# Optimization experiments

Hardware: AMD Instinct MI355X
Metric: run time of the kernel (lower is better)

Reference implementation:

```python
import jax, jax.numpy as jnp
import numpy as np

N_HEADS = 8


def setup_inputs() -> dict:
    key = jax.random.key(0)
    qkv = jax.random.normal(key, (4, 1536, 2048), dtype=jnp.float32)
    return {"qkv": qkv}


def reference(qkv):
    bs, width, length = qkv.shape
    assert width % (3 * N_HEADS) == 0
    ch = width // (3 * N_HEADS)
    q, k, v = jnp.split(qkv, 3, axis=1)            # each [bs, H*C, T]
    scale = 1.0 / (ch ** 0.25)                      # 1/sqrt(sqrt(ch)) applied to both q and k
    q = (q * scale).reshape(bs * N_HEADS, ch, length)
    k = (k * scale).reshape(bs * N_HEADS, ch, length)
    v = v.reshape(bs * N_HEADS, ch, length)
    weight = jnp.einsum('bct,bcs->bts', q, k)       # [bs*H, T, T]
    weight = jax.nn.softmax(weight.astype(jnp.float32), axis=-1).astype(weight.dtype)
    a = jnp.einsum('bts,bcs->bct', weight, v)       # [bs*H, C, T]
    return a.reshape(bs, -1, length)
```

## Files before the change

kernel.cpp:

```cpp
#include <hip/hip_runtime.h>


typedef _Float16 half8  __attribute__((ext_vector_type(8)));
typedef _Float16 half4  __attribute__((ext_vector_type(4)));
typedef float    floatx4 __attribute__((ext_vector_type(4)));

constexpr int T    = 2048;
constexpr int TQ   = 128;
constexpr int TS   = 64;
constexpr int LDK  = 72;
constexpr int LDV  = 72;
constexpr int KHALF  = TS * LDK;
constexpr int SMEM_H = KHALF + 64 * LDV;
constexpr int NIT  = T / TS;
constexpr float QSCALE = 0.125f * 1.44269504088896340736f;

__device__ __forceinline__ half4 pack4(float a, float b, float c, float d) {
    half4 r;
    r[0] = (_Float16)a; r[1] = (_Float16)b;
    r[2] = (_Float16)c; r[3] = (_Float16)d;
    return r;
}

__global__ __launch_bounds__(512, 4)
void qkv_attn_kernel(const float* __restrict__ qkv, float* __restrict__ out) {
    __shared__ __align__(16) _Float16 smem[2][SMEM_H];

    const int tid  = threadIdx.x;
    const int wave = tid >> 6;
    const int lane = tid & 63;
    const int n16  = lane & 15;
    const int g    = lane >> 4;
    const int h    = wave >> 2;
    const int qg   = wave & 3;

    const int bx = blockIdx.x;
    const int hd = bx & 31;
    const int qt = bx >> 5;
    const int b  = hd >> 3;
    const int hh = hd & 7;
    const int q0 = qt * TQ;

    const float* __restrict__ qbase = qkv + (size_t)(b * 1536 + hh * 64) * T;
    const float* __restrict__ kbase = qkv + (size_t)(b * 1536 + 512 + hh * 64) * T;
    const float* __restrict__ vbase = qkv + (size_t)(b * 1536 + 1024 + hh * 64) * T;
    float* __restrict__ obase = out + (size_t)(b * 512 + hh * 64) * T;

    const bool kstage = (wave < 4);
    const int ptid = tid & 255;
    const int ks   = ((ptid >> 6) << 4) | (ptid & 15);
    const int kc4  = ((ptid >> 4) & 3) << 2;
    const int vc   = ptid >> 4;
    const int vt   = ptid & 15;
    const int vcol = 32 * (vt >> 3) + 8 * (vt & 3) + 4 * ((vt >> 2) & 1);

    float pre[16];
    auto prefetch = [&](int s0) {
        if (kstage) {
            const float* kg = kbase + s0 + ks;
#pragma unroll
            for (int i = 0; i < 4; ++i) {
                const int c = i * 16 + kc4;
#pragma unroll
                for (int j = 0; j < 4; ++j) pre[i * 4 + j] = kg[(c + j) * T];
            }
        } else {
            const float* vg = vbase + vc * T + s0 + vt * 4;
#pragma unroll
            for (int i = 0; i < 4; ++i) {
                const floatx4 vv = *(const floatx4*)&vg[i * 16 * T];
                pre[i * 4 + 0] = vv.x; pre[i * 4 + 1] = vv.y;
                pre[i * 4 + 2] = vv.z; pre[i * 4 + 3] = vv.w;
            }
        }
    };
    auto flush = [&](int buf) {
        if (kstage) {
            _Float16* kd = &smem[buf][ks * LDK];
#pragma unroll
            for (int i = 0; i < 4; ++i)
                *(half4*)&kd[i * 16 + kc4] =
                    pack4(pre[i * 4], pre[i * 4 + 1], pre[i * 4 + 2], pre[i * 4 + 3]);
        } else {
            _Float16* vd = &smem[buf][KHALF + vc * LDV + vcol];
#pragma unroll
            for (int i = 0; i < 4; ++i)
                *(half4*)&vd[i * 16 * LDV] =
                    pack4(pre[i * 4], pre[i * 4 + 1], pre[i * 4 + 2], pre[i * 4 + 3]);
        }
    };

    half8 bq[2][2];
    floatx4 oacc[4][2];
    float lsum[2];

#pragma unroll
    for (int qt2 = 0; qt2 < 2; ++qt2) {
        const int q = q0 + qg * 32 + qt2 * 16 + n16;
#pragma unroll
        for (int kcA = 0; kcA < 2; ++kcA)
#pragma unroll
            for (int j = 0; j < 8; ++j) {
                const int c = kcA * 32 + g * 8 + j;
                bq[qt2][kcA][j] = (_Float16)(qbase[c * T + q] * QSCALE);
            }
    }
#pragma unroll
    for (int mt = 0; mt < 4; ++mt)
#pragma unroll
        for (int qt2 = 0; qt2 < 2; ++qt2) oacc[mt][qt2] = (floatx4)(0.f);
    lsum[0] = 0.f; lsum[1] = 0.f;

    prefetch(0);
    flush(0);
    __syncthreads();

    for (int it = 0; it < NIT; ++it) {
        const int buf = it & 1;
        if (it + 1 < NIT) prefetch((it + 1) * TS);

        const _Float16* kb = &smem[buf][0];
        const _Float16* vb = &smem[buf][KHALF];

        floatx4 sacc[2][2];
#pragma unroll
        for (int sub = 0; sub < 2; ++sub) {
            const half8 ak0 = *(const half8*)&kb[((h * 2 + sub) * 16 + n16) * LDK + g * 8];
            const half8 ak1 = *(const half8*)&kb[((h * 2 + sub) * 16 + n16) * LDK + 32 + g * 8];
#pragma unroll
            for (int qt2 = 0; qt2 < 2; ++qt2) {
                floatx4 acc = (floatx4)(0.f);
                acc = __builtin_amdgcn_mfma_f32_16x16x32_f16(ak0, bq[qt2][0], acc, 0, 0, 0);
                acc = __builtin_amdgcn_mfma_f32_16x16x32_f16(ak1, bq[qt2][1], acc, 0, 0, 0);
                sacc[qt2][sub] = acc;
            }
        }
        half8 av[4];
#pragma unroll
        for (int mt = 0; mt < 4; ++mt)
            av[mt] = *(const half8*)&vb[(mt * 16 + n16) * LDV + h * 32 + g * 8];
#pragma unroll
        for (int qt2 = 0; qt2 < 2; ++qt2) {
            float pv[8];
#pragma unroll
            for (int sub = 0; sub < 2; ++sub)
#pragma unroll
                for (int r = 0; r < 4; ++r)
                    pv[sub * 4 + r] = __builtin_amdgcn_exp2f(sacc[qt2][sub][r]);
            lsum[qt2] += ((pv[0] + pv[1]) + (pv[2] + pv[3]))
                       + ((pv[4] + pv[5]) + (pv[6] + pv[7]));
            half8 bp;
#pragma unroll
            for (int i = 0; i < 8; ++i) bp[i] = (_Float16)pv[i];
#pragma unroll
            for (int mt = 0; mt < 4; ++mt)
                oacc[mt][qt2] = __builtin_amdgcn_mfma_f32_16x16x32_f16(
                    av[mt], bp, oacc[mt][qt2], 0, 0, 0);
        }

        if (it + 1 < NIT) flush(buf ^ 1);
        __syncthreads();
    }

    float* red = (float*)&smem[0][0];
    const int rbase = (qg * 64 + lane) * 36;
    if (h == 1) {
#pragma unroll
        for (int qt2 = 0; qt2 < 2; ++qt2)
#pragma unroll
            for (int mt = 0; mt < 4; ++mt)
                *(floatx4*)&red[rbase + (qt2 * 4 + mt) * 4] = oacc[mt][qt2];
        red[rbase + 32] = lsum[0];
        red[rbase + 33] = lsum[1];
    }
    __syncthreads();
    if (h == 0) {
#pragma unroll
        for (int qt2 = 0; qt2 < 2; ++qt2)
#pragma unroll
            for (int mt = 0; mt < 4; ++mt)
                oacc[mt][qt2] += *(const floatx4*)&red[rbase + (qt2 * 4 + mt) * 4];
        lsum[0] += red[rbase + 32];
        lsum[1] += red[rbase + 33];
#pragma unroll
        for (int qt2 = 0; qt2 < 2; ++qt2) {
            float l = lsum[qt2];
            l += __shfl_xor(l, 16);
            l += __shfl_xor(l, 32);
            const float linv = 1.0f / l;
            const int tcol = q0 + qg * 32 + qt2 * 16 + n16;
#pragma unroll
            for (int mt = 0; mt < 4; ++mt)
#pragma unroll
                for (int r = 0; r < 4; ++r)
                    obase[(mt * 16 + g * 4 + r) * T + tcol] = oacc[mt][qt2][r] * linv;
        }
    }
}

extern "C" void kernel_launch(void* const* d_in, const int* in_sizes, int n_in,
                              void* d_out, int out_size, void* d_ws, size_t ws_size,
                              hipStream_t stream) {
    const float* qkv = (const float*)d_in[0];
    float* out = (float*)d_out;
    qkv_attn_kernel<<<dim3(512), dim3(512), 0, stream>>>(qkv, out);
}
```

Before: 124.3 us.

## Split keys four ways per block with 1024 threads and tree-reduce partials

Doubles the block to 1024 threads and the key tile to 128, so four wave groups each handle a quarter of every key tile for the same 128 queries. Partial outputs and row sums are then combined in a two-step shared-memory tree with an XOR swizzle. Staging now loads from global and writes straight into the other shared buffer, replacing the register prefetch and the flush after compute, and V fragments are loaded inside the MFMA loop to save registers. The aim is more waves in flight to hide latency, but it costs extra reduction barriers, global-load latency exposed before compute, and register pressure from the launch bounds.

```diff
diff --git a/kernel.cpp b/kernel.cpp
--- a/kernel.cpp
+++ b/kernel.cpp
@@ -7,12 +7,13 @@
 
 constexpr int T    = 2048;
 constexpr int TQ   = 128;
-constexpr int TS   = 64;
+constexpr int TS   = 128;
 constexpr int LDK  = 72;
-constexpr int LDV  = 72;
+constexpr int LDV  = 136;
 constexpr int KHALF  = TS * LDK;
 constexpr int SMEM_H = KHALF + 64 * LDV;
 constexpr int NIT  = T / TS;
+constexpr int LBASE = 16384;
 constexpr float QSCALE = 0.125f * 1.44269504088896340736f;
 
 __device__ __forceinline__ half4 pack4(float a, float b, float c, float d) {
@@ -22,7 +23,7 @@
     return r;
 }
 
-__global__ __launch_bounds__(512, 4)
+__global__ __launch_bounds__(1024, 8)
 void qkv_attn_kernel(const float* __restrict__ qkv, float* __restrict__ out) {
     __shared__ __align__(16) _Float16 smem[2][SMEM_H];
 
@@ -31,8 +32,8 @@
     const int lane = tid & 63;
     const int n16  = lane & 15;
     const int g    = lane >> 4;
-    const int h    = wave >> 2;
     const int qg   = wave & 3;
+    const int sq   = wave >> 2;
 
     const int bx = blockIdx.x;
     const int hd = bx & 31;
@@ -46,47 +47,35 @@
     const float* __restrict__ vbase = qkv + (size_t)(b * 1536 + 1024 + hh * 64) * T;
     float* __restrict__ obase = out + (size_t)(b * 512 + hh * 64) * T;
 
-    const bool kstage = (wave < 4);
-    const int ptid = tid & 255;
+    const bool kstage = (wave < 8);
+    const int ptid = tid & 511;
     const int ks   = ((ptid >> 6) << 4) | (ptid & 15);
     const int kc4  = ((ptid >> 4) & 3) << 2;
-    const int vc   = ptid >> 4;
-    const int vt   = ptid & 15;
+    const int vc   = ptid >> 5;
+    const int vt   = ptid & 31;
     const int vcol = 32 * (vt >> 3) + 8 * (vt & 3) + 4 * ((vt >> 2) & 1);
 
-    float pre[16];
-    auto prefetch = [&](int s0) {
+    auto stage = [&](int buf, int s0) {
         if (kstage) {
+            _Float16* kd = &smem[buf][ks * LDK];
             const float* kg = kbase + s0 + ks;
 #pragma unroll
             for (int i = 0; i < 4; ++i) {
                 const int c = i * 16 + kc4;
-#pragma unroll
-                for (int j = 0; j < 4; ++j) pre[i * 4 + j] = kg[(c + j) * T];
+                const float f0 = kg[(c + 0) * T];
+                const float f1 = kg[(c + 1) * T];
+                const float f2 = kg[(c + 2) * T];
+                const float f3 = kg[(c + 3) * T];
+                *(half4*)&kd[c] = pack4(f0, f1, f2, f3);
             }
         } else {
             const float* vg = vbase + vc * T + s0 + vt * 4;
+            _Float16* vd = &smem[buf][KHALF + vc * LDV + vcol];
 #pragma unroll
             for (int i = 0; i < 4; ++i) {
                 const floatx4 vv = *(const floatx4*)&vg[i * 16 * T];
-                pre[i * 4 + 0] = vv.x; pre[i * 4 + 1] = vv.y;
-                pre[i * 4 + 2] = vv.z; pre[i * 4 + 3] = vv.w;
-            }
-        }
-    };
-    auto flush = [&](int buf) {
-        if (kstage) {
-            _Float16* kd = &smem[buf][ks * LDK];
-#pragma unroll
-            for (int i = 0; i < 4; ++i)
-                *(half4*)&kd[i * 16 + kc4] =
-                    pack4(pre[i * 4], pre[i * 4 + 1], pre[i * 4 + 2], pre[i * 4 + 3]);
-        } else {
-            _Float16* vd = &smem[buf][KHALF + vc * LDV + vcol];
-#pragma unroll
-            for (int i = 0; i < 4; ++i)
-                *(half4*)&vd[i * 16 * LDV] =
-                    pack4(pre[i * 4], pre[i * 4 + 1], pre[i * 4 + 2], pre[i * 4 + 3]);
+                *(half4*)&vd[i * 16 * LDV] = pack4(vv.x, vv.y, vv.z, vv.w);
+            }
         }
     };
 
@@ -111,13 +100,12 @@
         for (int qt2 = 0; qt2 < 2; ++qt2) oacc[mt][qt2] = (floatx4)(0.f);
     lsum[0] = 0.f; lsum[1] = 0.f;
 
-    prefetch(0);
-    flush(0);
+    stage(0, 0);
     __syncthreads();
 
     for (int it = 0; it < NIT; ++it) {
         const int buf = it & 1;
-        if (it + 1 < NIT) prefetch((it + 1) * TS);
+        if (it + 1 < NIT) stage(buf ^ 1, (it + 1) * TS);
 
         const _Float16* kb = &smem[buf][0];
         const _Float16* vb = &smem[buf][KHALF];
@@ -125,8 +113,9 @@
         floatx4 sacc[2][2];
 #pragma unroll
         for (int sub = 0; sub < 2; ++sub) {
-            const half8 ak0 = *(const half8*)&kb[((h * 2 + sub) * 16 + n16) * LDK + g * 8];
-            const half8 ak1 = *(const half8*)&kb[((h * 2 + sub) * 16 + n16) * LDK + 32 + g * 8];
+            const int srow = (sq * 2 + sub) * 16 + n16;
+            const half8 ak0 = *(const half8*)&kb[srow * LDK + g * 8];
+            const half8 ak1 = *(const half8*)&kb[srow * LDK + 32 + g * 8];
 #pragma unroll
             for (int qt2 = 0; qt2 < 2; ++qt2) {
                 floatx4 acc = (floatx4)(0.f);
@@ -135,10 +124,6 @@
                 sacc[qt2][sub] = acc;
             }
         }
-        half8 av[4];
-#pragma unroll
-        for (int mt = 0; mt < 4; ++mt)
-            av[mt] = *(const half8*)&vb[(mt * 16 + n16) * LDV + h * 32 + g * 8];
 #pragma unroll
         for (int qt2 = 0; qt2 < 2; ++qt2) {
             float pv[8];
@@ -153,35 +138,63 @@
 #pragma unroll
             for (int i = 0; i < 8; ++i) bp[i] = (_Float16)pv[i];
 #pragma unroll
-            for (int mt = 0; mt < 4; ++mt)
+            for (int mt = 0; mt < 4; ++mt) {
+                const half8 av = *(const half8*)&vb[(mt * 16 + n16) * LDV + sq * 32 + g * 8];
                 oacc[mt][qt2] = __builtin_amdgcn_mfma_f32_16x16x32_f16(
-                    av[mt], bp, oacc[mt][qt2], 0, 0, 0);
-        }
-
-        if (it + 1 < NIT) flush(buf ^ 1);
+                    av, bp, oacc[mt][qt2], 0, 0, 0);
+            }
+        }
+
         __syncthreads();
     }
 
     float* red = (float*)&smem[0][0];
-    const int rbase = (qg * 64 + lane) * 36;
-    if (h == 1) {
-#pragma unroll
-        for (int qt2 = 0; qt2 < 2; ++qt2)
-#pragma unroll
-            for (int mt = 0; mt < 4; ++mt)
-                *(floatx4*)&red[rbase + (qt2 * 4 + mt) * 4] = oacc[mt][qt2];
-        red[rbase + 32] = lsum[0];
-        red[rbase + 33] = lsum[1];
-    }
-    __syncthreads();
-    if (h == 0) {
-#pragma unroll
-        for (int qt2 = 0; qt2 < 2; ++qt2)
-#pragma unroll
-            for (int mt = 0; mt < 4; ++mt)
-                oacc[mt][qt2] += *(const floatx4*)&red[rbase + (qt2 * 4 + mt) * 4];
-        lsum[0] += red[rbase + 32];
-        lsum[1] += red[rbase + 33];
+    if (sq >= 2) {
+        const int slot = ((sq - 2) * 4 + qg) * 64 + lane;
+        const int rbase = slot * 32, sw = slot & 7;
+#pragma unroll
+        for (int qt2 = 0; qt2 < 2; ++qt2)
+#pragma unroll
+            for (int mt = 0; mt < 4; ++mt)
+                *(floatx4*)&red[rbase + (((qt2 * 4 + mt) ^ sw) << 2)] = oacc[mt][qt2];
+        red[LBASE + slot * 2]     = lsum[0];
+        red[LBASE + slot * 2 + 1] = lsum[1];
+    }
+    __syncthreads();
+    if (sq < 2) {
+        const int slot = (sq * 4 + qg) * 64 + lane;
+        const int rbase = slot * 32, sw = slot & 7;
+#pragma unroll
+        for (int qt2 = 0; qt2 < 2; ++qt2)
+#pragma unroll
+            for (int mt = 0; mt < 4; ++mt)
+                oacc[mt][qt2] += *(const floatx4*)&red[rbase + (((qt2 * 4 + mt) ^ sw) << 2)];
+        lsum[0] += red[LBASE + slot * 2];
+        lsum[1] += red[LBASE + slot * 2 + 1];
+    }
+    __syncthreads();
+    if (sq == 1) {
+        const int slot = qg * 64 + lane;
+        const int rbase = slot * 32, sw = slot & 7;
+#pragma unroll
+        for (int qt2 = 0; qt2 < 2; ++qt2)
+#pragma unroll
+            for (int mt = 0; mt < 4; ++mt)
+                *(floatx4*)&red[rbase + (((qt2 * 4 + mt) ^ sw) << 2)] = oacc[mt][qt2];
+        red[LBASE + slot * 2]     = lsum[0];
+        red[LBASE + slot * 2 + 1] = lsum[1];
+    }
+    __syncthreads();
+    if (sq == 0) {
+        const int slot = qg * 64 + lane;
+        const int rbase = slot * 32, sw = slot & 7;
+#pragma unroll
+        for (int qt2 = 0; qt2 < 2; ++qt2)
+#pragma unroll
+            for (int mt = 0; mt < 4; ++mt)
+                oacc[mt][qt2] += *(const floatx4*)&red[rbase + (((qt2 * 4 + mt) ^ sw) << 2)];
+        lsum[0] += red[LBASE + slot * 2];
+        lsum[1] += red[LBASE + slot * 2 + 1];
 #pragma unroll
         for (int qt2 = 0; qt2 < 2; ++qt2) {
             float l = lsum[qt2];
@@ -203,5 +216,5 @@
                               hipStream_t stream) {
     const float* qkv = (const float*)d_in[0];
     float* out = (float*)d_out;
-    qkv_attn_kernel<<<dim3(512), dim3(512), 0, stream>>>(qkv, out);
+    qkv_attn_kernel<<<dim3(512), dim3(1024), 0, stream>>>(qkv, out);
 }
```

Measured after the change: 449.7 us. 3.62x slower.

## Pre-convert K and V to swizzled fp16 and stream them via direct-to-LDS loads

Applied to the files above, without the earlier changes.

Two new pre-pass kernels convert K (transposed) and V from fp32 into fp16 workspace buffers, each stored in an XOR-swizzled layout that matches the MFMA fragment reads. The attention kernel then loads each tile with global_load_lds straight into shared memory, replacing the register prefetch, convert and flush path. This halves the bytes the attention kernel reads for K and V, which are re-read by every query tile, and removes the conversion work from its inner loop. In exchange it adds two extra kernel launches and a write and read of the fp16 workspace.

```diff
diff --git a/kernel.cpp b/kernel.cpp
--- a/kernel.cpp
+++ b/kernel.cpp
@@ -2,92 +2,89 @@
 
 
 typedef _Float16 half8  __attribute__((ext_vector_type(8)));
-typedef _Float16 half4  __attribute__((ext_vector_type(4)));
 typedef float    floatx4 __attribute__((ext_vector_type(4)));
 
-constexpr int T    = 2048;
-constexpr int TQ   = 128;
-constexpr int TS   = 64;
-constexpr int LDK  = 72;
-constexpr int LDV  = 72;
-constexpr int KHALF  = TS * LDK;
-constexpr int SMEM_H = KHALF + 64 * LDV;
-constexpr int NIT  = T / TS;
+constexpr int T = 2048;
+constexpr int HEAD_HALVES = 64 * 2048;
 constexpr float QSCALE = 0.125f * 1.44269504088896340736f;
 
-__device__ __forceinline__ half4 pack4(float a, float b, float c, float d) {
-    half4 r;
-    r[0] = (_Float16)a; r[1] = (_Float16)b;
-    r[2] = (_Float16)c; r[3] = (_Float16)d;
-    return r;
+__global__ __launch_bounds__(256) void cvtK(const float* __restrict__ qkv,
+                                            _Float16* __restrict__ KT) {
+    const int t  = blockIdx.x * 256 + threadIdx.x;
+    const int hd = t >> 11, s = t & 2047;
+    const int b = hd >> 3, hh = hd & 7;
+    const float* kcol = qkv + (size_t)(b * 1536 + 512 + hh * 64) * T + s;
+    _Float16* row = KT + (size_t)hd * HEAD_HALVES + s * 64;
+    const int sw = s & 7;
+#pragma unroll
+    for (int k = 0; k < 8; ++k) {
+        half8 v;
+#pragma unroll
+        for (int j = 0; j < 8; ++j) v[j] = (_Float16)kcol[(size_t)(k * 8 + j) * T];
+        *(half8*)&row[(k ^ sw) * 8] = v;
+    }
+}
+
+__global__ __launch_bounds__(256) void cvtV(const float* __restrict__ qkv,
+                                            _Float16* __restrict__ VH) {
+    const int bc = blockIdx.x;
+    const int hd = bc >> 6, c = bc & 63;
+    const int b = hd >> 3, hh = hd & 7;
+    const float* vrow = qkv + (size_t)(b * 1536 + 1024 + hh * 64 + c) * T;
+    _Float16* orow = VH + (size_t)hd * HEAD_HALVES + c * 2048;
+    const int tile = threadIdx.x >> 3, pos = threadIdx.x & 7;
+    const int k6 = pos ^ (c & 7);
+    const int sq = k6 >> 2, g = k6 & 3;
+    half8 v;
+#pragma unroll
+    for (int j = 0; j < 8; ++j) {
+        const int tl = sq * 32 + 16 * (j >> 2) + 4 * g + (j & 3);
+        v[j] = (_Float16)vrow[tile * 64 + tl];
+    }
+    *(half8*)&orow[tile * 64 + pos * 8] = v;
 }
 
 __global__ __launch_bounds__(512, 4)
-void qkv_attn_kernel(const float* __restrict__ qkv, float* __restrict__ out) {
-    __shared__ __align__(16) _Float16 smem[2][SMEM_H];
+void qkv_attn_kernel(const float* __restrict__ qkv,
+                     const _Float16* __restrict__ KT,
+                     const _Float16* __restrict__ VH,
+                     float* __restrict__ out) {
+    __shared__ __align__(16) unsigned char raw[36864];
+    _Float16* lds = (_Float16*)raw;
 
     const int tid  = threadIdx.x;
     const int wave = tid >> 6;
     const int lane = tid & 63;
     const int n16  = lane & 15;
     const int g    = lane >> 4;
-    const int h    = wave >> 2;
     const int qg   = wave & 3;
+    const int sh   = wave >> 2;
 
     const int bx = blockIdx.x;
     const int hd = bx & 31;
     const int qt = bx >> 5;
     const int b  = hd >> 3;
     const int hh = hd & 7;
-    const int q0 = qt * TQ;
+    const int q0 = qt * 128;
 
     const float* __restrict__ qbase = qkv + (size_t)(b * 1536 + hh * 64) * T;
-    const float* __restrict__ kbase = qkv + (size_t)(b * 1536 + 512 + hh * 64) * T;
-    const float* __restrict__ vbase = qkv + (size_t)(b * 1536 + 1024 + hh * 64) * T;
     float* __restrict__ obase = out + (size_t)(b * 512 + hh * 64) * T;
-
-    const bool kstage = (wave < 4);
-    const int ptid = tid & 255;
-    const int ks   = ((ptid >> 6) << 4) | (ptid & 15);
-    const int kc4  = ((ptid >> 4) & 3) << 2;
-    const int vc   = ptid >> 4;
-    const int vt   = ptid & 15;
-    const int vcol = 32 * (vt >> 3) + 8 * (vt & 3) + 4 * ((vt >> 2) & 1);
-
-    float pre[16];
-    auto prefetch = [&](int s0) {
-        if (kstage) {
-            const float* kg = kbase + s0 + ks;
-#pragma unroll
-            for (int i = 0; i < 4; ++i) {
-                const int c = i * 16 + kc4;
-#pragma unroll
-                for (int j = 0; j < 4; ++j) pre[i * 4 + j] = kg[(c + j) * T];
-            }
-        } else {
-            const float* vg = vbase + vc * T + s0 + vt * 4;
-#pragma unroll
-            for (int i = 0; i < 4; ++i) {
-                const floatx4 vv = *(const floatx4*)&vg[i * 16 * T];
-                pre[i * 4 + 0] = vv.x; pre[i * 4 + 1] = vv.y;
-                pre[i * 4 + 2] = vv.z; pre[i * 4 + 3] = vv.w;
-            }
-        }
-    };
-    auto flush = [&](int buf) {
-        if (kstage) {
-            _Float16* kd = &smem[buf][ks * LDK];
-#pragma unroll
-            for (int i = 0; i < 4; ++i)
-                *(half4*)&kd[i * 16 + kc4] =
-                    pack4(pre[i * 4], pre[i * 4 + 1], pre[i * 4 + 2], pre[i * 4 + 3]);
-        } else {
-            _Float16* vd = &smem[buf][KHALF + vc * LDV + vcol];
-#pragma unroll
-            for (int i = 0; i < 4; ++i)
-                *(half4*)&vd[i * 16 * LDV] =
-                    pack4(pre[i * 4], pre[i * 4 + 1], pre[i * 4 + 2], pre[i * 4 + 3]);
-        }
+    const _Float16* kth = KT + (size_t)hd * HEAD_HALVES;
+    const _Float16* vhh = VH + (size_t)hd * HEAD_HALVES;
+
+    const int vrow_l = wave * 8 + (lane >> 3);
+    const int vpos_l = lane & 7;
+    auto issue = [&](int buf, int it) {
+        const _Float16* kg = kth + it * 4096 + wave * 512 + lane * 8;
+        _Float16* kd = lds + buf * 4096 + wave * 512;
+        __builtin_amdgcn_global_load_lds(
+            (const __attribute__((address_space(1))) void*)kg,
+            (__attribute__((address_space(3))) void*)kd, 16, 0, 0);
+        const _Float16* vg = vhh + (size_t)vrow_l * 2048 + it * 64 + vpos_l * 8;
+        _Float16* vd = lds + 8192 + buf * 4096 + wave * 512;
+        __builtin_amdgcn_global_load_lds(
+            (const __attribute__((address_space(1))) void*)vg,
+            (__attribute__((address_space(3))) void*)vd, 16, 0, 0);
     };
 
     half8 bq[2][2];
@@ -111,22 +108,23 @@
         for (int qt2 = 0; qt2 < 2; ++qt2) oacc[mt][qt2] = (floatx4)(0.f);
     lsum[0] = 0.f; lsum[1] = 0.f;
 
-    prefetch(0);
-    flush(0);
+    issue(0, 0);
     __syncthreads();
 
-    for (int it = 0; it < NIT; ++it) {
+    for (int it = 0; it < 32; ++it) {
         const int buf = it & 1;
-        if (it + 1 < NIT) prefetch((it + 1) * TS);
-
-        const _Float16* kb = &smem[buf][0];
-        const _Float16* vb = &smem[buf][KHALF];
+        if (it + 1 < 32) issue(buf ^ 1, it + 1);
+
+        const _Float16* kb = lds + buf * 4096;
+        const _Float16* vb = lds + 8192 + buf * 4096;
 
         floatx4 sacc[2][2];
 #pragma unroll
         for (int sub = 0; sub < 2; ++sub) {
-            const half8 ak0 = *(const half8*)&kb[((h * 2 + sub) * 16 + n16) * LDK + g * 8];
-            const half8 ak1 = *(const half8*)&kb[((h * 2 + sub) * 16 + n16) * LDK + 32 + g * 8];
+            const int srow = sh * 32 + sub * 16 + n16;
+            const int sw = srow & 7;
+            const half8 ak0 = *(const half8*)&kb[srow * 64 + ((g ^ sw) * 8)];
+            const half8 ak1 = *(const half8*)&kb[srow * 64 + (((g ^ sw) ^ 4) * 8)];
 #pragma unroll
             for (int qt2 = 0; qt2 < 2; ++qt2) {
                 floatx4 acc = (floatx4)(0.f);
@@ -137,8 +135,11 @@
         }
         half8 av[4];
 #pragma unroll
-        for (int mt = 0; mt < 4; ++mt)
-            av[mt] = *(const half8*)&vb[(mt * 16 + n16) * LDV + h * 32 + g * 8];
+        for (int mt = 0; mt < 4; ++mt) {
+            const int c = mt * 16 + n16;
+            const int posv = (sh * 4 + g) ^ (c & 7);
+            av[mt] = *(const half8*)&vb[c * 64 + posv * 8];
+        }
 #pragma unroll
         for (int qt2 = 0; qt2 < 2; ++qt2) {
             float pv[8];
@@ -158,13 +159,12 @@
                     av[mt], bp, oacc[mt][qt2], 0, 0, 0);
         }
 
-        if (it + 1 < NIT) flush(buf ^ 1);
         __syncthreads();
     }
 
-    float* red = (float*)&smem[0][0];
+    float* red = (float*)raw;
     const int rbase = (qg * 64 + lane) * 36;
-    if (h == 1) {
+    if (sh == 1) {
 #pragma unroll
         for (int qt2 = 0; qt2 < 2; ++qt2)
 #pragma unroll
@@ -174,7 +174,7 @@
         red[rbase + 33] = lsum[1];
     }
     __syncthreads();
-    if (h == 0) {
+    if (sh == 0) {
 #pragma unroll
         for (int qt2 = 0; qt2 < 2; ++qt2)
 #pragma unroll
@@ -203,5 +203,9 @@
                               hipStream_t stream) {
     const float* qkv = (const float*)d_in[0];
     float* out = (float*)d_out;
-    qkv_attn_kernel<<<dim3(512), dim3(512), 0, stream>>>(qkv, out);
-}
+    _Float16* KT = (_Float16*)d_ws;
+    _Float16* VH = KT + (size_t)32 * HEAD_HALVES;
+    cvtK<<<dim3(256), dim3(256), 0, stream>>>(qkv, KT);
+    cvtV<<<dim3(2048), dim3(256), 0, stream>>>(qkv, VH);
+    qkv_attn_kernel<<<dim3(512), dim3(512), 0, stream>>>(qkv, KT, VH, out);
+}
```

After: 127.7 us. 1.03x slower.
